# Kernel tuning notes

Hardware: AMD Instinct MI355X
Metric: run time of the kernel (lower is better)

Reference implementation:

```python
import jax, jax.numpy as jnp
import numpy as np

NOISE_STD = 0.1
TOP_K = 2

def setup_inputs() -> dict:
    key = jax.random.key(0)
    k1, k2, k3, k4 = jax.random.split(key, 4)
    B, S, H = 4, 4096, 2048
    E, SE, NS = 64, 64, 10
    x = jax.random.normal(k1, (B, S, H), dtype=jnp.float32)
    scale_embeddings = jax.random.normal(k2, (NS, SE), dtype=jnp.float32)
    # nn.Linear(H+SE, E, bias=False) weight: [E, H+SE]
    router_w = jax.random.normal(k3, (E, H + SE), dtype=jnp.float32) / np.sqrt(H + SE).astype(np.float32)
    # pre-sampled standard-normal noise (training path), scaled by NOISE_STD inside reference
    noise = jax.random.normal(k4, (B, S, E), dtype=jnp.float32)
    return {"x": x, "scale_embeddings": scale_embeddings, "router_w": router_w,
            "noise": noise, "scale_idx": 3}

def reference(x, scale_embeddings, router_w, noise, scale_idx):
    B, S, _ = x.shape
    # scale_idx is not None branch: lookup one scale embedding, broadcast over tokens
    emb = scale_embeddings[scale_idx]                      # [SE]
    emb = jnp.broadcast_to(emb, (B, S, emb.shape[-1]))     # [B,S,SE]
    x_with_scale = jnp.concatenate([x, emb], axis=-1)      # [B,S,H+SE]
    # router: bias-free linear projection to expert logits
    router_logits = jnp.einsum('bsd,ed->bse', x_with_scale, router_w)
    router_logits = router_logits + noise * NOISE_STD      # training noise injection
    routing_probs = jax.nn.softmax(router_logits, axis=-1)  # [B,S,E]
    routing_weights, selected_experts = jax.lax.top_k(routing_probs, TOP_K)
    routing_weights = routing_weights / routing_weights.sum(axis=-1, keepdims=True)
    # scatter normalized weights into dense dispatch tensor [B,S,E]
    dispatch = (jax.nn.one_hot(selected_experts, routing_probs.shape[-1],
                               dtype=routing_probs.dtype)
                * routing_weights[..., None]).sum(axis=-2)
    return dispatch
```

## Files before the change

### kernel.cpp

```cpp
#include <hip/hip_runtime.h>
#include <hip/hip_bf16.h>
#include <math.h>
#include <stdint.h>


#define H_DIM 2048
#define K_TOTAL 2112
#define E_DIM 64
#define SE_DIM 64
#define NSTEP 64
#define TPB 32
#define NBLOCKS (16384 / TPB)
#define STEP_BYTES (12 * 1024)
#define SET_BYTES (16 * 1024)
#define WP_TOTAL (NSTEP * STEP_BYTES)
#define MINS(v) ((v) < NSTEP ? (v) : (NSTEP - 1))

typedef float  f32x4 __attribute__((ext_vector_type(4)));
typedef short  s16x8 __attribute__((ext_vector_type(8)));
typedef unsigned int u32x4 __attribute__((ext_vector_type(4)));

typedef uint32_t __attribute__((address_space(1))) gu32_t;
typedef uint32_t __attribute__((address_space(3))) lu32_t;
__device__ __forceinline__ void gload_lds16(const void* g, void* l) {
    __builtin_amdgcn_global_load_lds((const gu32_t*)g, (lu32_t*)l, 16, 0, 0);
}

__device__ __forceinline__ unsigned short bf16_rne(float f) {
    uint32_t u = __float_as_uint(f);
    return (unsigned short)((u + 0x7FFFu + ((u >> 16) & 1u)) >> 16);
}
__device__ __forceinline__ float bf16_f32(unsigned short h) {
    return __uint_as_float(((uint32_t)h) << 16);
}
__device__ __forceinline__ uint32_t bits_of_bf2(__hip_bfloat162 h) {
    uint32_t u; __builtin_memcpy(&u, &h, 4); return u;
}

__global__ void prep_kernel(const float* __restrict__ W,
                            const float* __restrict__ se,
                            const int* __restrict__ sidx,
                            unsigned short* __restrict__ Wp,
                            float* __restrict__ tail) {
    if (blockIdx.x == 64) {
        int e = threadIdx.x;
        if (e < 64) {
            const float* emb = se + (*sidx) * SE_DIM;
            float t = 0.f;
            for (int j = 0; j < SE_DIM; ++j)
                t = fmaf(emb[j], W[(size_t)e * K_TOTAL + H_DIM + j], t);
            tail[e] = t;
        }
        return;
    }
    int item = blockIdx.x * 256 + threadIdx.x;
    int lane = item & 63;
    int nt   = (item >> 6) & 3;
    int s    = item >> 8;
    int e     = nt * 16 + (lane & 15);
    int kbase = s * 32 + (lane >> 4) * 8;
    const float* wr = W + (size_t)e * K_TOTAL + kbase;
    unsigned short p0[8], p1[8], p2[8];
    #pragma unroll
    for (int j = 0; j < 8; ++j) {
        float v = wr[j];
        unsigned short a0 = bf16_rne(v);
        float r1 = v - bf16_f32(a0);
        unsigned short a1 = bf16_rne(r1);
        float r2 = r1 - bf16_f32(a1);
        p0[j] = a0; p1[j] = a1; p2[j] = bf16_rne(r2);
    }
    size_t rec = (size_t)s * 12 + nt * 3;
    unsigned short* d0 = Wp + (rec + 0) * 512 + lane * 8;
    unsigned short* d1 = Wp + (rec + 1) * 512 + lane * 8;
    unsigned short* d2 = Wp + (rec + 2) * 512 + lane * 8;
    #pragma unroll
    for (int j = 0; j < 8; ++j) { d0[j] = p0[j]; d1[j] = p1[j]; d2[j] = p2[j]; }
}

__device__ __forceinline__ void split3(const float4 fa, const float4 fb,
                                       s16x8& P0, s16x8& P1, s16x8& P2) {
    float f[8] = {fa.x, fa.y, fa.z, fa.w, fb.x, fb.y, fb.z, fb.w};
    uint32_t d0[4], d1[4], d2[4];
    #pragma unroll
    for (int p = 0; p < 4; ++p) {
        float v0 = f[2 * p], v1 = f[2 * p + 1];
        uint32_t u0 = bits_of_bf2(__float22bfloat162_rn(make_float2(v0, v1)));
        float r0 = v0 - __uint_as_float(u0 << 16);
        float r1 = v1 - __uint_as_float(u0 & 0xffff0000u);
        uint32_t u1 = bits_of_bf2(__float22bfloat162_rn(make_float2(r0, r1)));
        float s0 = r0 - __uint_as_float(u1 << 16);
        float s1 = r1 - __uint_as_float(u1 & 0xffff0000u);
        uint32_t u2 = bits_of_bf2(__float22bfloat162_rn(make_float2(s0, s1)));
        d0[p] = u0; d1[p] = u1; d2[p] = u2;
    }
    u32x4 q0 = {d0[0], d0[1], d0[2], d0[3]};
    u32x4 q1 = {d1[0], d1[1], d1[2], d1[3]};
    u32x4 q2 = {d2[0], d2[1], d2[2], d2[3]};
    __builtin_memcpy(&P0, &q0, 16);
    __builtin_memcpy(&P1, &q1, 16);
    __builtin_memcpy(&P2, &q2, 16);
}

__launch_bounds__(512, 4)
__global__ void router_kernel(const float* __restrict__ x,
                              const unsigned char* __restrict__ Wp,
                              const float* __restrict__ tail_g,
                              const float* __restrict__ noise,
                              float* __restrict__ out) {
    __shared__ __align__(16) unsigned char S[4][SET_BYTES];
    __shared__ float4 cand[4][TPB];
    __shared__ float4 res[TPB];

    const int tid  = threadIdx.x;
    const int lane = tid & 63;
    const int wave = __builtin_amdgcn_readfirstlane(tid >> 6);
    const int mt   = wave >> 2;
    const int g    = wave & 3;
    const int tok0 = blockIdx.x * TPB;
    const int row  = lane & 15;
    const int quad = lane >> 4;
    const int c    = row;

    const char* s1; size_t str1;
    if (tid < 256) {
        int st = tid >> 3, sp = tid & 7;
        s1 = (const char*)(x + (size_t)(tok0 + st) * H_DIM + ((sp ^ (st & 7)) << 2));
        str1 = 128;
    } else {
        s1 = (const char*)Wp + (size_t)(tid - 256) * 16;
        str1 = STEP_BYTES;
    }
    const char* s2 = (const char*)Wp + (size_t)(tid + 256) * 16;
    const int d1 = tid * 16;
    const int d2 = tid * 16 + 8192;

    const int abase = (mt * 16 + row) * 128;
    const int aoff0 = abase + (((quad * 2)     ^ (row & 7)) << 4);
    const int aoff1 = abase + (((quad * 2 + 1) ^ (row & 7)) << 4);
    const int boff  = 4096 + g * 3072 + lane * 16;

    f32x4 acc = {0.f, 0.f, 0.f, 0.f};

    #define ISSUE_SET(s_, d_) do {                                  \
        gload_lds16(s1 + (size_t)(s_) * str1,       &S[d_][d1]);    \
        gload_lds16(s2 + (size_t)(s_) * STEP_BYTES, &S[d_][d2]);    \
    } while (0)

    ISSUE_SET(0, 0);
    ISSUE_SET(1, 1);
    ISSUE_SET(2, 2);

    for (int s = 0; s < NSTEP; ++s) {
        asm volatile("s_waitcnt vmcnt(4)\n\ts_barrier" ::: "memory");

        ISSUE_SET(MINS(s + 3), (s + 3) & 3);

        const unsigned char* sb = &S[s & 3][0];
        float4 a0 = *(const float4*)(sb + aoff0);
        float4 a1 = *(const float4*)(sb + aoff1);
        s16x8 A0, A1, A2;
        split3(a0, a1, A0, A1, A2);

        const unsigned char* bb = sb + boff;
        s16x8 B0 = *(const s16x8*)(bb);
        s16x8 B1 = *(const s16x8*)(bb + 1024);
        s16x8 B2 = *(const s16x8*)(bb + 2048);
        acc = __builtin_amdgcn_mfma_f32_16x16x32_bf16(A0, B0, acc, 0, 0, 0);
        acc = __builtin_amdgcn_mfma_f32_16x16x32_bf16(A0, B1, acc, 0, 0, 0);
        acc = __builtin_amdgcn_mfma_f32_16x16x32_bf16(A1, B0, acc, 0, 0, 0);
        acc = __builtin_amdgcn_mfma_f32_16x16x32_bf16(A0, B2, acc, 0, 0, 0);
        acc = __builtin_amdgcn_mfma_f32_16x16x32_bf16(A1, B1, acc, 0, 0, 0);
        acc = __builtin_amdgcn_mfma_f32_16x16x32_bf16(A2, B0, acc, 0, 0, 0);
    }
    #undef ISSUE_SET

    float tl = tail_g[g * 16 + c];
    #pragma unroll
    for (int r = 0; r < 4; ++r) {
        const int tlk = mt * 16 + quad * 4 + r;
        const float* nz = noise + (size_t)(tok0 + tlk) * E_DIM + g * 16;
        float v = acc[r] + tl + 0.1f * nz[c];
        float V1 = v, V2 = -3.4e38f;
        int   I1 = g * 16 + c, I2 = 0x7fffffff;
        #pragma unroll
        for (int m = 8; m; m >>= 1) {
            float o1 = __shfl_xor(V1, m, 64); int oi1 = __shfl_xor(I1, m, 64);
            float o2 = __shfl_xor(V2, m, 64); int oi2 = __shfl_xor(I2, m, 64);
            if (o1 > V1 || (o1 == V1 && oi1 < I1)) {
                float nv2; int ni2;
                if (V1 > o2 || (V1 == o2 && I1 < oi2)) { nv2 = V1; ni2 = I1; }
                else                                   { nv2 = o2; ni2 = oi2; }
                V1 = o1; I1 = oi1; V2 = nv2; I2 = ni2;
            } else {
                if (o1 > V2 || (o1 == V2 && oi1 < I2)) { V2 = o1; I2 = oi1; }
            }
        }
        if (c == r)
            cand[g][tlk] = make_float4(V1, __int_as_float(I1), V2, __int_as_float(I2));
    }
    __syncthreads();

    if (tid < TPB) {
        float4 q0 = cand[0][tid];
        float V1 = q0.x, V2 = q0.z;
        int   I1 = __float_as_int(q0.y), I2 = __float_as_int(q0.w);
        #pragma unroll
        for (int j = 1; j < 4; ++j) {
            float4 qj = cand[j][tid];
            float o1 = qj.x, o2 = qj.z;
            int  oi1 = __float_as_int(qj.y), oi2 = __float_as_int(qj.w);
            if (o1 > V1) {
                if (o2 > V1) { V2 = o2; I2 = oi2; }
                else         { V2 = V1; I2 = I1;  }
                V1 = o1; I1 = oi1;
            } else if (o1 > V2) {
                V2 = o1; I2 = oi1;
            }
        }
        float d   = expf(V2 - V1);
        float inv = 1.0f / (1.0f + d);
        res[tid] = make_float4(inv, __int_as_float(I1), d * inv, __int_as_float(I2));
    }
    __syncthreads();

    float4* outb = (float4*)out + (size_t)blockIdx.x * (TPB * E_DIM / 4);
    {
        int t = tid >> 4, cc = tid & 15;
        float4 rr = res[t];
        int ri1 = __float_as_int(rr.y), ri2 = __float_as_int(rr.w);
        int e = cc * 4;
        float4 o;
        o.x = (e + 0 == ri1) ? rr.x : (e + 0 == ri2) ? rr.z : 0.0f;
        o.y = (e + 1 == ri1) ? rr.x : (e + 1 == ri2) ? rr.z : 0.0f;
        o.z = (e + 2 == ri1) ? rr.x : (e + 2 == ri2) ? rr.z : 0.0f;
        o.w = (e + 3 == ri1) ? rr.x : (e + 3 == ri2) ? rr.z : 0.0f;
        outb[tid] = o;
    }
}

extern "C" void kernel_launch(void* const* d_in, const int* in_sizes, int n_in,
                              void* d_out, int out_size, void* d_ws, size_t ws_size,
                              hipStream_t stream) {
    const float* x     = (const float*)d_in[0];
    const float* se    = (const float*)d_in[1];
    const float* W     = (const float*)d_in[2];
    const float* noise = (const float*)d_in[3];
    const int*   sidx  = (const int*)d_in[4];
    float* out = (float*)d_out;

    unsigned short* Wp   = (unsigned short*)d_ws;
    float*          tail = (float*)((char*)d_ws + WP_TOTAL);

    hipLaunchKernelGGL(prep_kernel, dim3(65), dim3(256), 0, stream, W, se, sidx, Wp, tail);
    hipLaunchKernelGGL(router_kernel, dim3(NBLOCKS), dim3(512), 0, stream,
                       x, (const unsigned char*)Wp, tail, noise, out);
}
```

Measured before the change: 241.3 us.

## Have each wave compute all 64 experts so A-split is shared across groups

Changes the block from 512 threads handling 32 tokens (each wave one 16-expert group) to 256 threads handling 64 tokens, with each wave covering all four expert groups in four accumulators. The fp32-to-3xbf16 split of the x tile is now done once per wave instead of four times, and the weight tile in LDS is reused across twice as many tokens. The cross-group candidate merge through LDS and one barrier are removed, since top-2 is merged in registers. The costs are more registers per thread, a larger LDS footprint per block, and half as many blocks to fill the GPU.

```diff
diff --git a/kernel.cpp b/kernel.cpp
--- a/kernel.cpp
+++ b/kernel.cpp
@@ -9,10 +9,10 @@
 #define E_DIM 64
 #define SE_DIM 64
 #define NSTEP 64
-#define TPB 32
+#define TPB 64
 #define NBLOCKS (16384 / TPB)
 #define STEP_BYTES (12 * 1024)
-#define SET_BYTES (16 * 1024)
+#define SET_BYTES (20 * 1024)
 #define WP_TOTAL (NSTEP * STEP_BYTES)
 #define MINS(v) ((v) < NSTEP ? (v) : (NSTEP - 1))
 
@@ -102,49 +102,45 @@
     __builtin_memcpy(&P2, &q2, 16);
 }
 
-__launch_bounds__(512, 4)
+__launch_bounds__(256, 2)
 __global__ void router_kernel(const float* __restrict__ x,
                               const unsigned char* __restrict__ Wp,
                               const float* __restrict__ tail_g,
                               const float* __restrict__ noise,
                               float* __restrict__ out) {
     __shared__ __align__(16) unsigned char S[4][SET_BYTES];
-    __shared__ float4 cand[4][TPB];
     __shared__ float4 res[TPB];
 
     const int tid  = threadIdx.x;
     const int lane = tid & 63;
     const int wave = __builtin_amdgcn_readfirstlane(tid >> 6);
-    const int mt   = wave >> 2;
-    const int g    = wave & 3;
+    const int mt   = wave;
     const int tok0 = blockIdx.x * TPB;
     const int row  = lane & 15;
     const int quad = lane >> 4;
     const int c    = row;
 
-    const char* s1; size_t str1;
-    if (tid < 256) {
-        int st = tid >> 3, sp = tid & 7;
-        s1 = (const char*)(x + (size_t)(tok0 + st) * H_DIM + ((sp ^ (st & 7)) << 2));
-        str1 = 128;
-    } else {
-        s1 = (const char*)Wp + (size_t)(tid - 256) * 16;
-        str1 = STEP_BYTES;
-    }
-    const char* s2 = (const char*)Wp + (size_t)(tid + 256) * 16;
-    const int d1 = tid * 16;
-    const int d2 = tid * 16 + 8192;
+    const int st  = tid >> 3;
+    const int sp  = tid & 7;
+    const int swz = sp ^ (st & 7);
+    const float*         aA = x + (size_t)(tok0 + st) * H_DIM + swz * 4;
+    const unsigned char* bB = Wp + (size_t)tid * 16;
+    const int dA = tid * 16;
 
     const int abase = (mt * 16 + row) * 128;
     const int aoff0 = abase + (((quad * 2)     ^ (row & 7)) << 4);
     const int aoff1 = abase + (((quad * 2 + 1) ^ (row & 7)) << 4);
-    const int boff  = 4096 + g * 3072 + lane * 16;
-
-    f32x4 acc = {0.f, 0.f, 0.f, 0.f};
-
-    #define ISSUE_SET(s_, d_) do {                                  \
-        gload_lds16(s1 + (size_t)(s_) * str1,       &S[d_][d1]);    \
-        gload_lds16(s2 + (size_t)(s_) * STEP_BYTES, &S[d_][d2]);    \
+
+    f32x4 acc0 = {0.f, 0.f, 0.f, 0.f}, acc1 = acc0, acc2 = acc0, acc3 = acc0;
+
+    #define ISSUE_SET(s_, d_) do {                                      \
+        const float*         _a = aA + (size_t)(s_) * 32;               \
+        const unsigned char* _b = bB + (size_t)(s_) * STEP_BYTES;       \
+        gload_lds16(_a,              &S[d_][dA]);                       \
+        gload_lds16(_a + 32 * H_DIM, &S[d_][dA + 4096]);                \
+        gload_lds16(_b,              &S[d_][dA + 8192]);                \
+        gload_lds16(_b + 4096,       &S[d_][dA + 12288]);               \
+        gload_lds16(_b + 8192,       &S[d_][dA + 16384]);               \
     } while (0)
 
     ISSUE_SET(0, 0);
@@ -152,7 +148,7 @@
     ISSUE_SET(2, 2);
 
     for (int s = 0; s < NSTEP; ++s) {
-        asm volatile("s_waitcnt vmcnt(4)\n\ts_barrier" ::: "memory");
+        asm volatile("s_waitcnt vmcnt(10)\n\ts_barrier" ::: "memory");
 
         ISSUE_SET(MINS(s + 3), (s + 3) & 3);
 
@@ -162,27 +158,74 @@
         s16x8 A0, A1, A2;
         split3(a0, a1, A0, A1, A2);
 
-        const unsigned char* bb = sb + boff;
-        s16x8 B0 = *(const s16x8*)(bb);
-        s16x8 B1 = *(const s16x8*)(bb + 1024);
-        s16x8 B2 = *(const s16x8*)(bb + 2048);
-        acc = __builtin_amdgcn_mfma_f32_16x16x32_bf16(A0, B0, acc, 0, 0, 0);
-        acc = __builtin_amdgcn_mfma_f32_16x16x32_bf16(A0, B1, acc, 0, 0, 0);
-        acc = __builtin_amdgcn_mfma_f32_16x16x32_bf16(A1, B0, acc, 0, 0, 0);
-        acc = __builtin_amdgcn_mfma_f32_16x16x32_bf16(A0, B2, acc, 0, 0, 0);
-        acc = __builtin_amdgcn_mfma_f32_16x16x32_bf16(A1, B1, acc, 0, 0, 0);
-        acc = __builtin_amdgcn_mfma_f32_16x16x32_bf16(A2, B0, acc, 0, 0, 0);
+        const unsigned char* bb = sb + 8192 + lane * 16;
+        {
+            s16x8 B0 = *(const s16x8*)(bb);
+            s16x8 B1 = *(const s16x8*)(bb + 1024);
+            s16x8 B2 = *(const s16x8*)(bb + 2048);
+            acc0 = __builtin_amdgcn_mfma_f32_16x16x32_bf16(A0, B0, acc0, 0, 0, 0);
+            acc0 = __builtin_amdgcn_mfma_f32_16x16x32_bf16(A0, B1, acc0, 0, 0, 0);
+            acc0 = __builtin_amdgcn_mfma_f32_16x16x32_bf16(A1, B0, acc0, 0, 0, 0);
+            acc0 = __builtin_amdgcn_mfma_f32_16x16x32_bf16(A0, B2, acc0, 0, 0, 0);
+            acc0 = __builtin_amdgcn_mfma_f32_16x16x32_bf16(A1, B1, acc0, 0, 0, 0);
+            acc0 = __builtin_amdgcn_mfma_f32_16x16x32_bf16(A2, B0, acc0, 0, 0, 0);
+        }
+        {
+            s16x8 B0 = *(const s16x8*)(bb + 3072);
+            s16x8 B1 = *(const s16x8*)(bb + 4096);
+            s16x8 B2 = *(const s16x8*)(bb + 5120);
+            acc1 = __builtin_amdgcn_mfma_f32_16x16x32_bf16(A0, B0, acc1, 0, 0, 0);
+            acc1 = __builtin_amdgcn_mfma_f32_16x16x32_bf16(A0, B1, acc1, 0, 0, 0);
+            acc1 = __builtin_amdgcn_mfma_f32_16x16x32_bf16(A1, B0, acc1, 0, 0, 0);
+            acc1 = __builtin_amdgcn_mfma_f32_16x16x32_bf16(A0, B2, acc1, 0, 0, 0);
+            acc1 = __builtin_amdgcn_mfma_f32_16x16x32_bf16(A1, B1, acc1, 0, 0, 0);
+            acc1 = __builtin_amdgcn_mfma_f32_16x16x32_bf16(A2, B0, acc1, 0, 0, 0);
+        }
+        {
+            s16x8 B0 = *(const s16x8*)(bb + 6144);
+            s16x8 B1 = *(const s16x8*)(bb + 7168);
+            s16x8 B2 = *(const s16x8*)(bb + 8192);
+            acc2 = __builtin_amdgcn_mfma_f32_16x16x32_bf16(A0, B0, acc2, 0, 0, 0);
+            acc2 = __builtin_amdgcn_mfma_f32_16x16x32_bf16(A0, B1, acc2, 0, 0, 0);
+            acc2 = __builtin_amdgcn_mfma_f32_16x16x32_bf16(A1, B0, acc2, 0, 0, 0);
+            acc2 = __builtin_amdgcn_mfma_f32_16x16x32_bf16(A0, B2, acc2, 0, 0, 0);
+            acc2 = __builtin_amdgcn_mfma_f32_16x16x32_bf16(A1, B1, acc2, 0, 0, 0);
+            acc2 = __builtin_amdgcn_mfma_f32_16x16x32_bf16(A2, B0, acc2, 0, 0, 0);
+        }
+        {
+            s16x8 B0 = *(const s16x8*)(bb + 9216);
+            s16x8 B1 = *(const s16x8*)(bb + 10240);
+            s16x8 B2 = *(const s16x8*)(bb + 11264);
+            acc3 = __builtin_amdgcn_mfma_f32_16x16x32_bf16(A0, B0, acc3, 0, 0, 0);
+            acc3 = __builtin_amdgcn_mfma_f32_16x16x32_bf16(A0, B1, acc3, 0, 0, 0);
+            acc3 = __builtin_amdgcn_mfma_f32_16x16x32_bf16(A1, B0, acc3, 0, 0, 0);
+            acc3 = __builtin_amdgcn_mfma_f32_16x16x32_bf16(A0, B2, acc3, 0, 0, 0);
+            acc3 = __builtin_amdgcn_mfma_f32_16x16x32_bf16(A1, B1, acc3, 0, 0, 0);
+            acc3 = __builtin_amdgcn_mfma_f32_16x16x32_bf16(A2, B0, acc3, 0, 0, 0);
+        }
     }
     #undef ISSUE_SET
 
-    float tl = tail_g[g * 16 + c];
+    const float t0 = tail_g[c];
+    const float t1 = tail_g[16 + c];
+    const float t2 = tail_g[32 + c];
+    const float t3 = tail_g[48 + c];
     #pragma unroll
     for (int r = 0; r < 4; ++r) {
-        const int tlk = mt * 16 + quad * 4 + r;
-        const float* nz = noise + (size_t)(tok0 + tlk) * E_DIM + g * 16;
-        float v = acc[r] + tl + 0.1f * nz[c];
-        float V1 = v, V2 = -3.4e38f;
-        int   I1 = g * 16 + c, I2 = 0x7fffffff;
+        const int tl = mt * 16 + quad * 4 + r;
+        const float* nz = noise + (size_t)(tok0 + tl) * E_DIM;
+        float v0 = acc0[r] + t0 + 0.1f * nz[c];
+        float v1 = acc1[r] + t1 + 0.1f * nz[16 + c];
+        float v2 = acc2[r] + t2 + 0.1f * nz[32 + c];
+        float v3 = acc3[r] + t3 + 0.1f * nz[48 + c];
+        float V1 = v0, V2 = -3.4e38f;
+        int   I1 = c,  I2 = 0x7fffffff;
+        if (v1 > V1)      { V2 = V1; I2 = I1; V1 = v1; I1 = 16 + c; }
+        else if (v1 > V2) { V2 = v1; I2 = 16 + c; }
+        if (v2 > V1)      { V2 = V1; I2 = I1; V1 = v2; I1 = 32 + c; }
+        else if (v2 > V2) { V2 = v2; I2 = 32 + c; }
+        if (v3 > V1)      { V2 = V1; I2 = I1; V1 = v3; I1 = 48 + c; }
+        else if (v3 > V2) { V2 = v3; I2 = 48 + c; }
         #pragma unroll
         for (int m = 8; m; m >>= 1) {
             float o1 = __shfl_xor(V1, m, 64); int oi1 = __shfl_xor(I1, m, 64);
@@ -196,37 +239,19 @@
                 if (o1 > V2 || (o1 == V2 && oi1 < I2)) { V2 = o1; I2 = oi1; }
             }
         }
-        if (c == r)
-            cand[g][tlk] = make_float4(V1, __int_as_float(I1), V2, __int_as_float(I2));
+        if (c == r) {
+            float d   = expf(V2 - V1);
+            float inv = 1.0f / (1.0f + d);
+            res[tl] = make_float4(inv, __int_as_float(I1), d * inv, __int_as_float(I2));
+        }
     }
     __syncthreads();
 
-    if (tid < TPB) {
-        float4 q0 = cand[0][tid];
-        float V1 = q0.x, V2 = q0.z;
-        int   I1 = __float_as_int(q0.y), I2 = __float_as_int(q0.w);
-        #pragma unroll
-        for (int j = 1; j < 4; ++j) {
-            float4 qj = cand[j][tid];
-            float o1 = qj.x, o2 = qj.z;
-            int  oi1 = __float_as_int(qj.y), oi2 = __float_as_int(qj.w);
-            if (o1 > V1) {
-                if (o2 > V1) { V2 = o2; I2 = oi2; }
-                else         { V2 = V1; I2 = I1;  }
-                V1 = o1; I1 = oi1;
-            } else if (o1 > V2) {
-                V2 = o1; I2 = oi1;
-            }
-        }
-        float d   = expf(V2 - V1);
-        float inv = 1.0f / (1.0f + d);
-        res[tid] = make_float4(inv, __int_as_float(I1), d * inv, __int_as_float(I2));
-    }
-    __syncthreads();
-
     float4* outb = (float4*)out + (size_t)blockIdx.x * (TPB * E_DIM / 4);
-    {
-        int t = tid >> 4, cc = tid & 15;
+    #pragma unroll
+    for (int pp = 0; pp < 4; ++pp) {
+        int p = tid + pp * 256;
+        int t = p >> 4, cc = p & 15;
         float4 rr = res[t];
         int ri1 = __float_as_int(rr.y), ri2 = __float_as_int(rr.w);
         int e = cc * 4;
@@ -235,7 +260,7 @@
         o.y = (e + 1 == ri1) ? rr.x : (e + 1 == ri2) ? rr.z : 0.0f;
         o.z = (e + 2 == ri1) ? rr.x : (e + 2 == ri2) ? rr.z : 0.0f;
         o.w = (e + 3 == ri1) ? rr.x : (e + 3 == ri2) ? rr.z : 0.0f;
-        outb[tid] = o;
+        outb[p] = o;
     }
 }
 
@@ -253,6 +278,6 @@
     float*          tail = (float*)((char*)d_ws + WP_TOTAL);
 
     hipLaunchKernelGGL(prep_kernel, dim3(65), dim3(256), 0, stream, W, se, sidx, Wp, tail);
-    hipLaunchKernelGGL(router_kernel, dim3(NBLOCKS), dim3(512), 0, stream,
+    hipLaunchKernelGGL(router_kernel, dim3(NBLOCKS), dim3(256), 0, stream,
                        x, (const unsigned char*)Wp, tail, noise, out);
 }
```

Measured after the change: 247.2 us. 1.02x slower.

## Split K across blocks with LDS-resident weight slices and atomic logit reduction

Applied to the files above, without the earlier changes.

Replaces the single fused router kernel with a split-K GEMM: each block keeps one 256-wide K slice of the packed bf16 weights resident in LDS and streams x rows straight from global into registers, with software prefetching. Partial logits are reduced with float atomics into a zeroed workspace, and a separate finish kernel adds bias and noise and then does the top-2 selection and dispatch write. The aim is to stop re-streaming the weights through LDS for every token tile and to raise the number of MFMAs per weight load. In exchange it adds a memset, an extra kernel launch and a logits round-trip through global memory, many atomics, and non-deterministic float summation order, which can change top-k choices on near ties.

```diff
diff --git a/kernel.cpp b/kernel.cpp
--- a/kernel.cpp
+++ b/kernel.cpp
@@ -9,12 +9,15 @@
 #define E_DIM 64
 #define SE_DIM 64
 #define NSTEP 64
-#define TPB 32
-#define NBLOCKS (16384 / TPB)
+#define NKR 8
+#define KR_LEN 256
+#define KS_PER_KR 8
+#define TG_TOK 512
 #define STEP_BYTES (12 * 1024)
-#define SET_BYTES (16 * 1024)
 #define WP_TOTAL (NSTEP * STEP_BYTES)
-#define MINS(v) ((v) < NSTEP ? (v) : (NSTEP - 1))
+#define BSLICE_BYTES (KS_PER_KR * STEP_BYTES)
+#define LOGITS_OFF (WP_TOTAL + 256)
+#define LOGITS_BYTES (16384 * E_DIM * 4)
 
 typedef float  f32x4 __attribute__((ext_vector_type(4)));
 typedef short  s16x8 __attribute__((ext_vector_type(8)));
@@ -102,140 +105,171 @@
     __builtin_memcpy(&P2, &q2, 16);
 }
 
-__launch_bounds__(512, 4)
-__global__ void router_kernel(const float* __restrict__ x,
-                              const unsigned char* __restrict__ Wp,
-                              const float* __restrict__ tail_g,
-                              const float* __restrict__ noise,
-                              float* __restrict__ out) {
-    __shared__ __align__(16) unsigned char S[4][SET_BYTES];
-    __shared__ float4 cand[4][TPB];
-    __shared__ float4 res[TPB];
+__launch_bounds__(512, 2)
+__global__ void gemm_kernel(const float* __restrict__ x,
+                            const unsigned char* __restrict__ Wp,
+                            float* __restrict__ logits) {
+    __shared__ __align__(16) unsigned char Bs[BSLICE_BYTES];
 
     const int tid  = threadIdx.x;
     const int lane = tid & 63;
     const int wave = __builtin_amdgcn_readfirstlane(tid >> 6);
-    const int mt   = wave >> 2;
-    const int g    = wave & 3;
-    const int tok0 = blockIdx.x * TPB;
+    const int kr   = blockIdx.x >> 5;
+    const int tg   = blockIdx.x & 31;
     const int row  = lane & 15;
     const int quad = lane >> 4;
     const int c    = row;
 
-    const char* s1; size_t str1;
-    if (tid < 256) {
-        int st = tid >> 3, sp = tid & 7;
-        s1 = (const char*)(x + (size_t)(tok0 + st) * H_DIM + ((sp ^ (st & 7)) << 2));
-        str1 = 128;
-    } else {
-        s1 = (const char*)Wp + (size_t)(tid - 256) * 16;
-        str1 = STEP_BYTES;
-    }
-    const char* s2 = (const char*)Wp + (size_t)(tid + 256) * 16;
-    const int d1 = tid * 16;
-    const int d2 = tid * 16 + 8192;
-
-    const int abase = (mt * 16 + row) * 128;
-    const int aoff0 = abase + (((quad * 2)     ^ (row & 7)) << 4);
-    const int aoff1 = abase + (((quad * 2 + 1) ^ (row & 7)) << 4);
-    const int boff  = 4096 + g * 3072 + lane * 16;
-
-    f32x4 acc = {0.f, 0.f, 0.f, 0.f};
-
-    #define ISSUE_SET(s_, d_) do {                                  \
-        gload_lds16(s1 + (size_t)(s_) * str1,       &S[d_][d1]);    \
-        gload_lds16(s2 + (size_t)(s_) * STEP_BYTES, &S[d_][d2]);    \
-    } while (0)
-
-    ISSUE_SET(0, 0);
-    ISSUE_SET(1, 1);
-    ISSUE_SET(2, 2);
-
-    for (int s = 0; s < NSTEP; ++s) {
-        asm volatile("s_waitcnt vmcnt(4)\n\ts_barrier" ::: "memory");
-
-        ISSUE_SET(MINS(s + 3), (s + 3) & 3);
-
-        const unsigned char* sb = &S[s & 3][0];
-        float4 a0 = *(const float4*)(sb + aoff0);
-        float4 a1 = *(const float4*)(sb + aoff1);
-        s16x8 A0, A1, A2;
-        split3(a0, a1, A0, A1, A2);
-
-        const unsigned char* bb = sb + boff;
-        s16x8 B0 = *(const s16x8*)(bb);
-        s16x8 B1 = *(const s16x8*)(bb + 1024);
-        s16x8 B2 = *(const s16x8*)(bb + 2048);
-        acc = __builtin_amdgcn_mfma_f32_16x16x32_bf16(A0, B0, acc, 0, 0, 0);
-        acc = __builtin_amdgcn_mfma_f32_16x16x32_bf16(A0, B1, acc, 0, 0, 0);
-        acc = __builtin_amdgcn_mfma_f32_16x16x32_bf16(A1, B0, acc, 0, 0, 0);
-        acc = __builtin_amdgcn_mfma_f32_16x16x32_bf16(A0, B2, acc, 0, 0, 0);
-        acc = __builtin_amdgcn_mfma_f32_16x16x32_bf16(A1, B1, acc, 0, 0, 0);
-        acc = __builtin_amdgcn_mfma_f32_16x16x32_bf16(A2, B0, acc, 0, 0, 0);
-    }
-    #undef ISSUE_SET
-
-    float tl = tail_g[g * 16 + c];
-    #pragma unroll
-    for (int r = 0; r < 4; ++r) {
-        const int tlk = mt * 16 + quad * 4 + r;
-        const float* nz = noise + (size_t)(tok0 + tlk) * E_DIM + g * 16;
-        float v = acc[r] + tl + 0.1f * nz[c];
-        float V1 = v, V2 = -3.4e38f;
-        int   I1 = g * 16 + c, I2 = 0x7fffffff;
+    {
+        const unsigned char* bsrc = Wp + (size_t)kr * BSLICE_BYTES + tid * 16;
         #pragma unroll
-        for (int m = 8; m; m >>= 1) {
-            float o1 = __shfl_xor(V1, m, 64); int oi1 = __shfl_xor(I1, m, 64);
-            float o2 = __shfl_xor(V2, m, 64); int oi2 = __shfl_xor(I2, m, 64);
-            if (o1 > V1 || (o1 == V1 && oi1 < I1)) {
-                float nv2; int ni2;
-                if (V1 > o2 || (V1 == o2 && I1 < oi2)) { nv2 = V1; ni2 = I1; }
-                else                                   { nv2 = o2; ni2 = oi2; }
-                V1 = o1; I1 = oi1; V2 = nv2; I2 = ni2;
-            } else {
-                if (o1 > V2 || (o1 == V2 && oi1 < I2)) { V2 = o1; I2 = oi1; }
-            }
-        }
-        if (c == r)
-            cand[g][tlk] = make_float4(V1, __int_as_float(I1), V2, __int_as_float(I2));
-    }
-    __syncthreads();
-
-    if (tid < TPB) {
-        float4 q0 = cand[0][tid];
-        float V1 = q0.x, V2 = q0.z;
-        int   I1 = __float_as_int(q0.y), I2 = __float_as_int(q0.w);
-        #pragma unroll
-        for (int j = 1; j < 4; ++j) {
-            float4 qj = cand[j][tid];
-            float o1 = qj.x, o2 = qj.z;
-            int  oi1 = __float_as_int(qj.y), oi2 = __float_as_int(qj.w);
-            if (o1 > V1) {
-                if (o2 > V1) { V2 = o2; I2 = oi2; }
-                else         { V2 = V1; I2 = I1;  }
-                V1 = o1; I1 = oi1;
-            } else if (o1 > V2) {
-                V2 = o1; I2 = oi1;
-            }
-        }
-        float d   = expf(V2 - V1);
-        float inv = 1.0f / (1.0f + d);
-        res[tid] = make_float4(inv, __int_as_float(I1), d * inv, __int_as_float(I2));
-    }
-    __syncthreads();
-
-    float4* outb = (float4*)out + (size_t)blockIdx.x * (TPB * E_DIM / 4);
-    {
-        int t = tid >> 4, cc = tid & 15;
-        float4 rr = res[t];
-        int ri1 = __float_as_int(rr.y), ri2 = __float_as_int(rr.w);
-        int e = cc * 4;
+        for (int i = 0; i < 12; ++i)
+            gload_lds16(bsrc + i * 8192, &Bs[tid * 16 + i * 8192]);
+        asm volatile("s_waitcnt vmcnt(0)" ::: "memory");
+        __syncthreads();
+    }
+
+    const float* ap = x + (size_t)(tg * TG_TOK + wave * 64 + row) * H_DIM
+                        + kr * KR_LEN + quad * 8;
+    f32x4 acc0 = {0.f, 0.f, 0.f, 0.f}, acc1 = acc0, acc2 = acc0, acc3 = acc0;
+
+    #define A_ADDR(J) (ap + (size_t)((J) >> 3) * (16 * H_DIM) + ((J) & 7) * 32)
+    #define ISSUE(J, VA, VB) do {                                  \
+        const float* _p = A_ADDR(J);                               \
+        VA = *(const float4*)_p;                                   \
+        VB = *(const float4*)(_p + 4);                             \
+    } while (0)
+
+    #define FLUSH(MT) do {                                                  \
+        int tokb = tg * TG_TOK + wave * 64 + (MT) * 16 + quad * 4;          \
+        float* lg = logits + (size_t)tokb * E_DIM + c;                      \
+        _Pragma("unroll")                                                   \
+        for (int r = 0; r < 4; ++r) {                                       \
+            atomicAdd(lg + r * E_DIM +  0, acc0[r]);                        \
+            atomicAdd(lg + r * E_DIM + 16, acc1[r]);                        \
+            atomicAdd(lg + r * E_DIM + 32, acc2[r]);                        \
+            atomicAdd(lg + r * E_DIM + 48, acc3[r]);                        \
+        }                                                                   \
+        f32x4 _z = {0.f, 0.f, 0.f, 0.f};                                    \
+        acc0 = _z; acc1 = _z; acc2 = _z; acc3 = _z;                         \
+    } while (0)
+
+    #define COMPUTE(J, VA, VB) do {                                         \
+        s16x8 A0, A1, A2;                                                   \
+        split3(VA, VB, A0, A1, A2);                                         \
+        const unsigned char* _bb = &Bs[((J) & 7) * STEP_BYTES + lane * 16]; \
+        {                                                                   \
+            s16x8 B0 = *(const s16x8*)(_bb);                                \
+            s16x8 B1 = *(const s16x8*)(_bb + 1024);                         \
+            s16x8 B2 = *(const s16x8*)(_bb + 2048);                         \
+            acc0 = __builtin_amdgcn_mfma_f32_16x16x32_bf16(A0, B0, acc0, 0, 0, 0); \
+            acc0 = __builtin_amdgcn_mfma_f32_16x16x32_bf16(A0, B1, acc0, 0, 0, 0); \
+            acc0 = __builtin_amdgcn_mfma_f32_16x16x32_bf16(A1, B0, acc0, 0, 0, 0); \
+            acc0 = __builtin_amdgcn_mfma_f32_16x16x32_bf16(A0, B2, acc0, 0, 0, 0); \
+            acc0 = __builtin_amdgcn_mfma_f32_16x16x32_bf16(A1, B1, acc0, 0, 0, 0); \
+            acc0 = __builtin_amdgcn_mfma_f32_16x16x32_bf16(A2, B0, acc0, 0, 0, 0); \
+        }                                                                   \
+        {                                                                   \
+            s16x8 B0 = *(const s16x8*)(_bb + 3072);                         \
+            s16x8 B1 = *(const s16x8*)(_bb + 4096);                         \
+            s16x8 B2 = *(const s16x8*)(_bb + 5120);                         \
+            acc1 = __builtin_amdgcn_mfma_f32_16x16x32_bf16(A0, B0, acc1, 0, 0, 0); \
+            acc1 = __builtin_amdgcn_mfma_f32_16x16x32_bf16(A0, B1, acc1, 0, 0, 0); \
+            acc1 = __builtin_amdgcn_mfma_f32_16x16x32_bf16(A1, B0, acc1, 0, 0, 0); \
+            acc1 = __builtin_amdgcn_mfma_f32_16x16x32_bf16(A0, B2, acc1, 0, 0, 0); \
+            acc1 = __builtin_amdgcn_mfma_f32_16x16x32_bf16(A1, B1, acc1, 0, 0, 0); \
+            acc1 = __builtin_amdgcn_mfma_f32_16x16x32_bf16(A2, B0, acc1, 0, 0, 0); \
+        }                                                                   \
+        {                                                                   \
+            s16x8 B0 = *(const s16x8*)(_bb + 6144);                         \
+            s16x8 B1 = *(const s16x8*)(_bb + 7168);                         \
+            s16x8 B2 = *(const s16x8*)(_bb + 8192);                         \
+            acc2 = __builtin_amdgcn_mfma_f32_16x16x32_bf16(A0, B0, acc2, 0, 0, 0); \
+            acc2 = __builtin_amdgcn_mfma_f32_16x16x32_bf16(A0, B1, acc2, 0, 0, 0); \
+            acc2 = __builtin_amdgcn_mfma_f32_16x16x32_bf16(A1, B0, acc2, 0, 0, 0); \
+            acc2 = __builtin_amdgcn_mfma_f32_16x16x32_bf16(A0, B2, acc2, 0, 0, 0); \
+            acc2 = __builtin_amdgcn_mfma_f32_16x16x32_bf16(A1, B1, acc2, 0, 0, 0); \
+            acc2 = __builtin_amdgcn_mfma_f32_16x16x32_bf16(A2, B0, acc2, 0, 0, 0); \
+        }                                                                   \
+        {                                                                   \
+            s16x8 B0 = *(const s16x8*)(_bb + 9216);                         \
+            s16x8 B1 = *(const s16x8*)(_bb + 10240);                        \
+            s16x8 B2 = *(const s16x8*)(_bb + 11264);                        \
+            acc3 = __builtin_amdgcn_mfma_f32_16x16x32_bf16(A0, B0, acc3, 0, 0, 0); \
+            acc3 = __builtin_amdgcn_mfma_f32_16x16x32_bf16(A0, B1, acc3, 0, 0, 0); \
+            acc3 = __builtin_amdgcn_mfma_f32_16x16x32_bf16(A1, B0, acc3, 0, 0, 0); \
+            acc3 = __builtin_amdgcn_mfma_f32_16x16x32_bf16(A0, B2, acc3, 0, 0, 0); \
+            acc3 = __builtin_amdgcn_mfma_f32_16x16x32_bf16(A1, B1, acc3, 0, 0, 0); \
+            acc3 = __builtin_amdgcn_mfma_f32_16x16x32_bf16(A2, B0, acc3, 0, 0, 0); \
+        }                                                                   \
+        if (((J) & 7) == 7) FLUSH((J) >> 3);                                \
+    } while (0)
+
+    float4 a0_, b0_, a1_, b1_, a2_, b2_;
+    ISSUE(0, a0_, b0_);
+    ISSUE(1, a1_, b1_);
+    #pragma unroll 1
+    for (int it = 0; it < 10; ++it) {
+        const int j = it * 3;
+        ISSUE(j + 2, a2_, b2_);
+        __builtin_amdgcn_sched_barrier(0);
+        COMPUTE(j, a0_, b0_);
+        ISSUE(j + 3, a0_, b0_);
+        __builtin_amdgcn_sched_barrier(0);
+        COMPUTE(j + 1, a1_, b1_);
+        ISSUE(j + 4, a1_, b1_);
+        __builtin_amdgcn_sched_barrier(0);
+        COMPUTE(j + 2, a2_, b2_);
+    }
+    COMPUTE(30, a0_, b0_);
+    COMPUTE(31, a1_, b1_);
+
+    #undef COMPUTE
+    #undef FLUSH
+    #undef ISSUE
+    #undef A_ADDR
+}
+
+__launch_bounds__(256, 4)
+__global__ void finish_kernel(const float* __restrict__ logits,
+                              const float* __restrict__ tail,
+                              const float* __restrict__ noise,
+                              float* __restrict__ out) {
+    const int t = blockIdx.x * 256 + threadIdx.x;
+    const float4* L4 = (const float4*)(logits + (size_t)t * E_DIM);
+    const float4* N4 = (const float4*)(noise  + (size_t)t * E_DIM);
+    const float4* T4 = (const float4*)tail;
+
+    float V1 = -3.4e38f, V2 = -3.4e38f;
+    int   I1 = 0x7fffffff, I2 = 0x7fffffff;
+    #define UPD(V, E) do {                                          \
+        float _v = (V); int _e = (E);                               \
+        if (_v > V1)      { V2 = V1; I2 = I1; V1 = _v; I1 = _e; }   \
+        else if (_v > V2) { V2 = _v; I2 = _e; }                     \
+    } while (0)
+    #pragma unroll
+    for (int i = 0; i < 16; ++i) {
+        float4 l = L4[i], n = N4[i], tl = T4[i];
+        UPD(l.x + tl.x + 0.1f * n.x, i * 4 + 0);
+        UPD(l.y + tl.y + 0.1f * n.y, i * 4 + 1);
+        UPD(l.z + tl.z + 0.1f * n.z, i * 4 + 2);
+        UPD(l.w + tl.w + 0.1f * n.w, i * 4 + 3);
+    }
+    #undef UPD
+    float d   = expf(V2 - V1);
+    float inv = 1.0f / (1.0f + d);
+    float w1 = inv, w2 = d * inv;
+
+    float4* O4 = (float4*)(out + (size_t)t * E_DIM);
+    #pragma unroll
+    for (int i = 0; i < 16; ++i) {
+        int e = i * 4;
         float4 o;
-        o.x = (e + 0 == ri1) ? rr.x : (e + 0 == ri2) ? rr.z : 0.0f;
-        o.y = (e + 1 == ri1) ? rr.x : (e + 1 == ri2) ? rr.z : 0.0f;
-        o.z = (e + 2 == ri1) ? rr.x : (e + 2 == ri2) ? rr.z : 0.0f;
-        o.w = (e + 3 == ri1) ? rr.x : (e + 3 == ri2) ? rr.z : 0.0f;
-        outb[tid] = o;
+        o.x = (e + 0 == I1) ? w1 : (e + 0 == I2) ? w2 : 0.0f;
+        o.y = (e + 1 == I1) ? w1 : (e + 1 == I2) ? w2 : 0.0f;
+        o.z = (e + 2 == I1) ? w1 : (e + 2 == I2) ? w2 : 0.0f;
+        o.w = (e + 3 == I1) ? w1 : (e + 3 == I2) ? w2 : 0.0f;
+        O4[i] = o;
     }
 }
 
@@ -249,10 +283,15 @@
     const int*   sidx  = (const int*)d_in[4];
     float* out = (float*)d_out;
 
-    unsigned short* Wp   = (unsigned short*)d_ws;
-    float*          tail = (float*)((char*)d_ws + WP_TOTAL);
-
-    hipLaunchKernelGGL(prep_kernel, dim3(65), dim3(256), 0, stream, W, se, sidx, Wp, tail);
-    hipLaunchKernelGGL(router_kernel, dim3(NBLOCKS), dim3(512), 0, stream,
-                       x, (const unsigned char*)Wp, tail, noise, out);
-}
+    unsigned short* Wp     = (unsigned short*)d_ws;
+    float*          tail   = (float*)((char*)d_ws + WP_TOTAL);
+    float*          logits = (float*)((char*)d_ws + LOGITS_OFF);
+
+    hipMemsetAsync(logits, 0, LOGITS_BYTES, stream);
+    hipLaunchKernelGGL(prep_kernel, dim3(65), dim3(256), 0, stream,
+                       W, se, sidx, Wp, tail);
+    hipLaunchKernelGGL(gemm_kernel, dim3(NKR * 32), dim3(512), 0, stream,
+                       x, (const unsigned char*)Wp, logits);
+    hipLaunchKernelGGL(finish_kernel, dim3(64), dim3(256), 0, stream,
+                       logits, tail, noise, out);
+}
```

Result: faster. 220.6 us (-8.6%).
